# Kernel tuning notes

Measured on AMD Instinct MI355X. Metric: run time of the kernel, lower is better.

The kernel has to match this reference:

```python
import jax, jax.numpy as jnp
import numpy as np

N_NODES = 50000
N_EDGES = 800000
D_IN = 128
D_OUT = 128
NUM_RELS = 100


def setup_inputs() -> dict:
    key = jax.random.key(0)
    k1, k2, k3, k4, k5, k6, k7 = jax.random.split(key, 7)
    h = jax.random.normal(k1, (N_NODES, D_IN), dtype=jnp.float32)
    W = jax.random.normal(k2, (D_IN, D_OUT), dtype=jnp.float32) * 0.05
    attn = jax.random.normal(k3, (2 * D_OUT,), dtype=jnp.float32) * 0.05
    rel_emb = jax.random.normal(k4, (NUM_RELS, 1), dtype=jnp.float32)
    src = jax.random.randint(k5, (N_EDGES,), 0, N_NODES, dtype=jnp.int32)
    dst = jax.random.randint(k6, (N_EDGES,), 0, N_NODES, dtype=jnp.int32)
    etype = jax.random.randint(k7, (N_EDGES,), 0, NUM_RELS, dtype=jnp.int32)
    return {"h": h, "W": W, "attn": attn, "rel_emb": rel_emb,
            "src": src, "dst": dst, "etype": etype}


def reference(h, W, attn, rel_emb, src, dst, etype):
    # h: [N, d_in], W: [d_in, d_out], attn: [2*d_out], rel_emb: [R, 1]
    # src/dst/etype: [E]
    N = h.shape[0]
    d = W.shape[1]
    # padding_idx=0 in nn.Embedding -> row 0 is zero
    rel_table = rel_emb.at[0].set(0.0)
    z = h @ W  # [N, d_out]
    # attn_fc([z_src, z_dst]) = z_src @ a_l + z_dst @ a_r (split the concat-linear)
    s_src = z @ attn[:d]  # [N]
    s_dst = z @ attn[d:]  # [N]
    e = jax.nn.leaky_relu(s_src[src] + s_dst[dst])  # [E], slope 0.01 as in torch
    # segment softmax over incoming edges of each dst node
    m = jax.ops.segment_max(e, dst, num_segments=N)  # [N]
    ex = jnp.exp(e - m[dst])  # [E]
    denom = jax.ops.segment_sum(ex, dst, num_segments=N)  # [N]
    alpha = ex / denom[dst]  # [E]
    coef = rel_table[etype, 0] * alpha  # [E]  (rel_alpha * alpha)
    # weighted sum of source messages per destination node
    out = jax.ops.segment_sum(coef[:, None] * z[src], dst, num_segments=N)  # [N, d_out]
    return out
```

## Files before the change

kernel.cpp:

```cpp
#include <hip/hip_runtime.h>

#define D 128
#define GROWS 64
#define SPLIT 8
#define NPP (256 / SPLIT)
#define MAXPART 1024

typedef __attribute__((ext_vector_type(8))) short short8;
typedef __attribute__((ext_vector_type(4))) float float4v;

__device__ __forceinline__ ushort f2bf(float x) {
    uint u = __float_as_uint(x);
    return (ushort)((u + 0x7FFFu + ((u >> 16) & 1u)) >> 16);
}
__device__ __forceinline__ float bf_lo(uint u) { return __uint_as_float(u << 16); }
__device__ __forceinline__ float bf_hi(uint u) { return __uint_as_float(u & 0xFFFF0000u); }

__global__ __launch_bounds__(256) void convW_kernel(
    const float* __restrict__ W, ushort* __restrict__ Wtg)
{
    int idx = blockIdx.x * 256 + threadIdx.x;
    int k = idx >> 7, n = idx & 127;
    Wtg[n * 128 + k] = f2bf(W[idx]);
}

__global__ __launch_bounds__(512) void gemm_mfma_kernel(
    const float* __restrict__ h, const ushort* __restrict__ Wtg,
    const float* __restrict__ attn, const int* __restrict__ dst,
    ushort* __restrict__ zb, float* __restrict__ s_src, float* __restrict__ s_dst,
    int* __restrict__ histm, int nhi, int N, int E, int nblocks)
{
    __shared__ ushort ht[GROWS * 136];
    __shared__ float psum_s[GROWS][2];
    __shared__ float psum_d[GROWS][2];
    __shared__ int histA[256];
    const int tid = threadIdx.x;
    const int base = blockIdx.x * GROWS;

#pragma unroll
    for (int it = 0; it < 4; ++it) {
        int idx = it * 512 + tid;
        int r = idx >> 5, c4 = (idx & 31) * 4;
        float4 v = make_float4(0.f, 0.f, 0.f, 0.f);
        if (base + r < N) v = *(const float4*)&h[(size_t)(base + r) * D + c4];
        ushort4 u = make_ushort4(f2bf(v.x), f2bf(v.y), f2bf(v.z), f2bf(v.w));
        *(ushort4*)&ht[r * 136 + c4] = u;
    }
    if (tid < 256) histA[tid] = 0;
    __syncthreads();

    const int lane = tid & 63;
    const int wave = tid >> 6;
    const int wr = wave >> 1;
    const int wc = wave & 1;
    const int col = lane & 15;
    const int quad = lane >> 4;
    const int wm = wr * 16;

    float4v acc[4];
#pragma unroll
    for (int nt = 0; nt < 4; ++nt) acc[nt] = (float4v)(0.f);

#pragma unroll
    for (int kc = 0; kc < 128; kc += 32) {
        short8 a = *(const short8*)&ht[(wm + col) * 136 + kc + quad * 8];
#pragma unroll
        for (int nt = 0; nt < 4; ++nt) {
            short8 b = *(const short8*)&Wtg[(wc * 64 + nt * 16 + col) * 128 + kc + quad * 8];
            acc[nt] = __builtin_amdgcn_mfma_f32_16x16x32_bf16(a, b, acc[nt], 0, 0, 0);
        }
    }
    __syncthreads();

    float ps[4] = {0.f, 0.f, 0.f, 0.f}, pd[4] = {0.f, 0.f, 0.f, 0.f};
#pragma unroll
    for (int nt = 0; nt < 4; ++nt) {
        float aL = attn[wc * 64 + nt * 16 + col];
        float aR = attn[D + wc * 64 + nt * 16 + col];
#pragma unroll
        for (int reg = 0; reg < 4; ++reg) {
            float v = acc[nt][reg];
            ps[reg] = fmaf(v, aL, ps[reg]);
            pd[reg] = fmaf(v, aR, pd[reg]);
            ht[(wm + quad * 4 + reg) * 136 + wc * 64 + nt * 16 + col] = f2bf(v);
        }
    }
#pragma unroll
    for (int reg = 0; reg < 4; ++reg) {
#pragma unroll
        for (int off = 1; off < 16; off <<= 1) {
            ps[reg] += __shfl_xor(ps[reg], off);
            pd[reg] += __shfl_xor(pd[reg], off);
        }
        if (col == 0) {
            int rl = wm + quad * 4 + reg;
            psum_s[rl][wc] = ps[reg];
            psum_d[rl][wc] = pd[reg];
        }
    }
    __syncthreads();

    if (tid < GROWS && base + tid < N) {
        s_src[base + tid] = psum_s[tid][0] + psum_s[tid][1];
        s_dst[base + tid] = psum_d[tid][0] + psum_d[tid][1];
    }

#pragma unroll
    for (int it = 0; it < 2; ++it) {
        int idx = it * 512 + tid;
        int r = idx >> 4, c8 = idx & 15;
        if (base + r < N)
            *(uint4*)&zb[(size_t)(base + r) * D + c8 * 8] = *(uint4*)&ht[r * 136 + c8 * 8];
    }

    const int cpb = (E + nblocks - 1) / nblocks;
    const int cs = blockIdx.x * cpb;
    const int ce = min(cs + cpb, E);
    for (int i = cs + tid; i < ce; i += 512)
        atomicAdd(&histA[dst[i] >> 8], 1);
    __syncthreads();
    if (tid < nhi) histm[blockIdx.x * nhi + tid] = histA[tid];
}

__global__ __launch_bounds__(64) void binB1_kernel(
    int* __restrict__ histm, int* __restrict__ colsum, int nhi, int nchunk)
{
    const int b = blockIdx.x;
    const int t = threadIdx.x;
    const int K = (nchunk + 63) / 64;
    int v[16];
    int s = 0;
#pragma unroll
    for (int j = 0; j < 16; ++j) {
        int c = t * K + j;
        v[j] = (j < K && c < nchunk) ? histm[c * nhi + b] : 0;
        s += v[j];
    }
    int incl = s;
#pragma unroll
    for (int off = 1; off < 64; off <<= 1) {
        int u = __shfl_up(incl, off);
        if (t >= off) incl += u;
    }
    int run = incl - s;
#pragma unroll
    for (int j = 0; j < 16; ++j) {
        int c = t * K + j;
        if (j < K && c < nchunk) { histm[c * nhi + b] = run; run += v[j]; }
    }
    if (t == 63) colsum[b] = incl;
}

__device__ __forceinline__ void scan_colsum_wave0(
    const int* __restrict__ colsum, int* sbase, int nhi, int lane)
{
    int v[4];
    int s = 0;
#pragma unroll
    for (int j = 0; j < 4; ++j) {
        int c = lane * 4 + j;
        v[j] = (c < nhi) ? colsum[c] : 0;
        s += v[j];
    }
    int incl = s;
#pragma unroll
    for (int off = 1; off < 64; off <<= 1) {
        int u = __shfl_up(incl, off);
        if (lane >= off) incl += u;
    }
    int run = incl - s;
#pragma unroll
    for (int j = 0; j < 4; ++j) {
        run += v[j];
        sbase[lane * 4 + j] = run;
    }
}

__global__ __launch_bounds__(256) void binC_kernel(
    const int* __restrict__ src, const int* __restrict__ dst,
    const int* __restrict__ etype, const int* __restrict__ histm,
    const int* __restrict__ colsum, uint* __restrict__ binned,
    int nhi, int E, int nchunk)
{
    __shared__ int sbase[256];
    __shared__ int cur[256];
    const int tid = threadIdx.x;
    if (tid < 64) scan_colsum_wave0(colsum, sbase, nhi, tid);
    __syncthreads();
    if (tid < nhi)
        cur[tid] = ((tid == 0) ? 0 : sbase[tid - 1]) + histm[blockIdx.x * nhi + tid];
    __syncthreads();
    const int cpb = (E + nchunk - 1) / nchunk;
    const int cs = blockIdx.x * cpb;
    const int ce = min(cs + cpb, E);
    for (int i = cs + tid; i < ce; i += 256) {
        int d = dst[i];
        int pos = atomicAdd(&cur[d >> 8], 1);
        binned[pos] = (uint)src[i] | ((uint)etype[i] << 16) | ((uint)(d & 255) << 23);
    }
}

__global__ __launch_bounds__(256) void aggD_kernel(
    const uint* __restrict__ zb32, const float* __restrict__ s_src,
    const float* __restrict__ s_dst, const int* __restrict__ colsum,
    const uint* __restrict__ binned, const float* __restrict__ rel_emb,
    float* __restrict__ out, int nhi, int N, int R)
{
    __shared__ float rel_l[128];
    __shared__ int sbase[256];
    __shared__ int hist[NPP];
    __shared__ int loff[NPP + 1];
    __shared__ int cur[NPP];
    __shared__ uint sE[MAXPART];
    const int tid = threadIdx.x;
    const int lane = tid & 63;
    const int wave = tid >> 6;

    if (tid < R) rel_l[tid] = (tid == 0) ? 0.f : rel_emb[tid];
    if (wave == 0) scan_colsum_wave0(colsum, sbase, nhi, lane);
    if (tid < NPP) hist[tid] = 0;
    __syncthreads();

    const int hi = blockIdx.x / SPLIT;
    const int part = blockIdx.x % SPLIT;
    const int bb = (hi == 0) ? 0 : sbase[hi - 1];
    const int be = sbase[hi];
    const int lobase = part * NPP;

    for (int i = bb + tid; i < be; i += 256) {
        int li = (int)((binned[i] >> 23) & 0xFF) - lobase;
        if ((unsigned)li < NPP) atomicAdd(&hist[li], 1);
    }
    __syncthreads();
    if (wave == 0 && lane < NPP) {
        int hc = hist[lane];
        int incl = hc;
#pragma unroll
        for (int off = 1; off < NPP; off <<= 1) {
            int u = __shfl_up(incl, off);
            if (lane >= off) incl += u;
        }
        loff[lane + 1] = incl;
        if (lane == 0) loff[0] = 0;
        cur[lane] = incl - hc;
    }
    __syncthreads();
    for (int i = bb + tid; i < be; i += 256) {
        uint pk = binned[i];
        int li = (int)((pk >> 23) & 0xFF) - lobase;
        if ((unsigned)li < NPP) {
            int pos = atomicAdd(&cur[li], 1);
            if (pos < MAXPART) sE[pos] = pk;
        }
    }
    __syncthreads();

    const int q = lane >> 4;
    const int ql = lane & 15;
    const int qid = wave * 4 + q;
    const int qb = q * 16;

    for (int nIdx = qid; nIdx < NPP; nIdx += 16) {
        const int d = hi * 256 + lobase + nIdx;
        if (d >= N) continue;
        const int st = loff[nIdx];
        const int en = loff[nIdx + 1];
        const float sdst = s_dst[d];

        float lpart = 0.f;
        float4 acc0 = make_float4(0.f, 0.f, 0.f, 0.f);
        float4 acc1 = make_float4(0.f, 0.f, 0.f, 0.f);

        for (int b2 = st; b2 < en; b2 += 16) {
            const int idx = b2 + ql;
            const bool valid = idx < en;
            const uint packed = valid ? sE[idx] : 0;
            const int srcv = (int)(packed & 0xFFFF);
            const int et = (int)((packed >> 16) & 0x7F);
            float w = 0.f;
            if (valid) {
                float x = s_src[srcv] + sdst;
                float e = (x > 0.f) ? x : 0.01f * x;
                float p = __expf(e);
                lpart += p;
                w = p * rel_l[et];
            }
            const int nv = min(16, en - b2);
            for (int j = 0; j < nv; j += 4) {
                const float w0 = __shfl(w, qb + j);
                const float w1 = __shfl(w, qb + j + 1);
                const float w2 = __shfl(w, qb + j + 2);
                const float w3 = __shfl(w, qb + j + 3);
                const int s0 = __shfl(srcv, qb + j);
                const int s1 = __shfl(srcv, qb + j + 1);
                const int s2 = __shfl(srcv, qb + j + 2);
                const int s3 = __shfl(srcv, qb + j + 3);
                const uint4 u0 = *(const uint4*)(zb32 + (size_t)s0 * 64 + ql * 4);
                const uint4 u1 = *(const uint4*)(zb32 + (size_t)s1 * 64 + ql * 4);
                const uint4 u2 = *(const uint4*)(zb32 + (size_t)s2 * 64 + ql * 4);
                const uint4 u3 = *(const uint4*)(zb32 + (size_t)s3 * 64 + ql * 4);
                acc0.x = fmaf(w0, bf_lo(u0.x), acc0.x);
                acc0.y = fmaf(w0, bf_hi(u0.x), acc0.y);
                acc0.z = fmaf(w0, bf_lo(u0.y), acc0.z);
                acc0.w = fmaf(w0, bf_hi(u0.y), acc0.w);
                acc1.x = fmaf(w0, bf_lo(u0.z), acc1.x);
                acc1.y = fmaf(w0, bf_hi(u0.z), acc1.y);
                acc1.z = fmaf(w0, bf_lo(u0.w), acc1.z);
                acc1.w = fmaf(w0, bf_hi(u0.w), acc1.w);
                acc0.x = fmaf(w1, bf_lo(u1.x), acc0.x);
                acc0.y = fmaf(w1, bf_hi(u1.x), acc0.y);
                acc0.z = fmaf(w1, bf_lo(u1.y), acc0.z);
                acc0.w = fmaf(w1, bf_hi(u1.y), acc0.w);
                acc1.x = fmaf(w1, bf_lo(u1.z), acc1.x);
                acc1.y = fmaf(w1, bf_hi(u1.z), acc1.y);
                acc1.z = fmaf(w1, bf_lo(u1.w), acc1.z);
                acc1.w = fmaf(w1, bf_hi(u1.w), acc1.w);
                acc0.x = fmaf(w2, bf_lo(u2.x), acc0.x);
                acc0.y = fmaf(w2, bf_hi(u2.x), acc0.y);
                acc0.z = fmaf(w2, bf_lo(u2.y), acc0.z);
                acc0.w = fmaf(w2, bf_hi(u2.y), acc0.w);
                acc1.x = fmaf(w2, bf_lo(u2.z), acc1.x);
                acc1.y = fmaf(w2, bf_hi(u2.z), acc1.y);
                acc1.z = fmaf(w2, bf_lo(u2.w), acc1.z);
                acc1.w = fmaf(w2, bf_hi(u2.w), acc1.w);
                acc0.x = fmaf(w3, bf_lo(u3.x), acc0.x);
                acc0.y = fmaf(w3, bf_hi(u3.x), acc0.y);
                acc0.z = fmaf(w3, bf_lo(u3.y), acc0.z);
                acc0.w = fmaf(w3, bf_hi(u3.y), acc0.w);
                acc1.x = fmaf(w3, bf_lo(u3.z), acc1.x);
                acc1.y = fmaf(w3, bf_hi(u3.z), acc1.y);
                acc1.z = fmaf(w3, bf_lo(u3.w), acc1.z);
                acc1.w = fmaf(w3, bf_hi(u3.w), acc1.w);
            }
        }

        float l = lpart;
#pragma unroll
        for (int off = 8; off; off >>= 1) l += __shfl_xor(l, off);

        const float inv = (l > 0.f) ? 1.0f / l : 0.f;
        float* orow = out + (size_t)d * D + ql * 8;
        *(float4*)orow       = make_float4(acc0.x * inv, acc0.y * inv, acc0.z * inv, acc0.w * inv);
        *(float4*)(orow + 4) = make_float4(acc1.x * inv, acc1.y * inv, acc1.z * inv, acc1.w * inv);
    }
}

extern "C" void kernel_launch(void* const* d_in, const int* in_sizes, int n_in,
                              void* d_out, int out_size, void* d_ws, size_t ws_size,
                              hipStream_t stream)
{
    const float* h    = (const float*)d_in[0];
    const float* W    = (const float*)d_in[1];
    const float* attn = (const float*)d_in[2];
    const float* rel  = (const float*)d_in[3];
    const int*   src  = (const int*)d_in[4];
    const int*   dst  = (const int*)d_in[5];
    const int*   et   = (const int*)d_in[6];
    float* out = (float*)d_out;

    const int N = in_sizes[0] / D;
    const int E = in_sizes[4];
    const int R = in_sizes[3];

    char* p = (char*)d_ws;
    auto alloc = [&](size_t bytes) {
        char* q = p;
        p += (bytes + 255) & ~(size_t)255;
        return q;
    };
    const int nhi     = (N + 255) / 256;
    const int gblocks = (N + GROWS - 1) / GROWS;

    ushort* zb     = (ushort*)alloc((size_t)N * D * sizeof(ushort));
    ushort* Wtg    = (ushort*)alloc((size_t)D * D * sizeof(ushort));
    float* ssrc    = (float*)alloc((size_t)N * sizeof(float));
    float* sdst    = (float*)alloc((size_t)N * sizeof(float));
    uint*  binned  = (uint*)alloc((size_t)E * sizeof(uint));
    int*   histm   = (int*)alloc((size_t)gblocks * nhi * sizeof(int));
    int*   colsum  = (int*)alloc((size_t)nhi * sizeof(int));

    convW_kernel<<<64, 256, 0, stream>>>(W, Wtg);
    gemm_mfma_kernel<<<gblocks, 512, 0, stream>>>(h, Wtg, attn, dst, zb, ssrc, sdst,
                                                  histm, nhi, N, E, gblocks);
    binB1_kernel<<<nhi, 64, 0, stream>>>(histm, colsum, nhi, gblocks);
    binC_kernel<<<gblocks, 256, 0, stream>>>(src, dst, et, histm, colsum, binned,
                                             nhi, E, gblocks);
    aggD_kernel<<<nhi * SPLIT, 256, 0, stream>>>((const uint*)zb, ssrc, sdst,
                                                 colsum, binned, rel, out, nhi, N, R);
}
```

Measured before the change: 162.1 us.

## Precompute edge softmax weights block-wide in LDS and deepen gather unroll

The aggregation kernel now computes each edge's exponentiated score and relation-scaled weight in a block-wide pass, storing weights in shared memory and accumulating per-node denominators with shared atomics. The per-node gather loop then reads precomputed weights and issues 8 independent row loads at a time instead of shuffling within 16-lane groups. SPLIT doubles to 16 so each quarter-wave owns exactly one destination node, and MAXPART halves. This aims to raise memory-level parallelism and drop shuffle overhead, but it launches more blocks that each rescan the same bin, and edge lists longer than MAXPART are truncated.

```diff
diff --git a/kernel.cpp b/kernel.cpp
--- a/kernel.cpp
+++ b/kernel.cpp
@@ -2,9 +2,9 @@
 
 #define D 128
 #define GROWS 64
-#define SPLIT 8
+#define SPLIT 16
 #define NPP (256 / SPLIT)
-#define MAXPART 1024
+#define MAXPART 512
 
 typedef __attribute__((ext_vector_type(8))) short short8;
 typedef __attribute__((ext_vector_type(4))) float float4v;
@@ -212,13 +212,16 @@
     __shared__ int loff[NPP + 1];
     __shared__ int cur[NPP];
     __shared__ uint sE[MAXPART];
+    __shared__ float sW[MAXPART];
+    __shared__ float sDst[NPP];
+    __shared__ float sDen[NPP];
     const int tid = threadIdx.x;
     const int lane = tid & 63;
     const int wave = tid >> 6;
 
     if (tid < R) rel_l[tid] = (tid == 0) ? 0.f : rel_emb[tid];
     if (wave == 0) scan_colsum_wave0(colsum, sbase, nhi, lane);
-    if (tid < NPP) hist[tid] = 0;
+    if (tid < NPP) { hist[tid] = 0; sDen[tid] = 0.f; }
     __syncthreads();
 
     const int hi = blockIdx.x / SPLIT;
@@ -226,6 +229,12 @@
     const int bb = (hi == 0) ? 0 : sbase[hi - 1];
     const int be = sbase[hi];
     const int lobase = part * NPP;
+    const int dbase = hi * 256 + lobase;
+
+    if (tid < NPP) {
+        int dd = dbase + tid;
+        sDst[tid] = (dd < N) ? s_dst[dd] : 0.f;
+    }
 
     for (int i = bb + tid; i < be; i += 256) {
         int li = (int)((binned[i] >> 23) & 0xFF) - lobase;
@@ -255,94 +264,65 @@
     }
     __syncthreads();
 
+    const int ne = min(loff[NPP], MAXPART);
+    for (int i = tid; i < ne; i += 256) {
+        uint pk = sE[i];
+        int srcv = (int)(pk & 0xFFFF);
+        int et = (int)((pk >> 16) & 0x7F);
+        int li = (int)((pk >> 23) & 0xFF) - lobase;
+        float x = s_src[srcv] + sDst[li];
+        float e = (x > 0.f) ? x : 0.01f * x;
+        float p = __expf(e);
+        sW[i] = p * rel_l[et];
+        atomicAdd(&sDen[li], p);
+    }
+    __syncthreads();
+
     const int q = lane >> 4;
     const int ql = lane & 15;
-    const int qid = wave * 4 + q;
-    const int qb = q * 16;
-
-    for (int nIdx = qid; nIdx < NPP; nIdx += 16) {
-        const int d = hi * 256 + lobase + nIdx;
-        if (d >= N) continue;
-        const int st = loff[nIdx];
-        const int en = loff[nIdx + 1];
-        const float sdst = s_dst[d];
-
-        float lpart = 0.f;
-        float4 acc0 = make_float4(0.f, 0.f, 0.f, 0.f);
-        float4 acc1 = make_float4(0.f, 0.f, 0.f, 0.f);
-
-        for (int b2 = st; b2 < en; b2 += 16) {
-            const int idx = b2 + ql;
-            const bool valid = idx < en;
-            const uint packed = valid ? sE[idx] : 0;
-            const int srcv = (int)(packed & 0xFFFF);
-            const int et = (int)((packed >> 16) & 0x7F);
-            float w = 0.f;
-            if (valid) {
-                float x = s_src[srcv] + sdst;
-                float e = (x > 0.f) ? x : 0.01f * x;
-                float p = __expf(e);
-                lpart += p;
-                w = p * rel_l[et];
-            }
-            const int nv = min(16, en - b2);
-            for (int j = 0; j < nv; j += 4) {
-                const float w0 = __shfl(w, qb + j);
-                const float w1 = __shfl(w, qb + j + 1);
-                const float w2 = __shfl(w, qb + j + 2);
-                const float w3 = __shfl(w, qb + j + 3);
-                const int s0 = __shfl(srcv, qb + j);
-                const int s1 = __shfl(srcv, qb + j + 1);
-                const int s2 = __shfl(srcv, qb + j + 2);
-                const int s3 = __shfl(srcv, qb + j + 3);
-                const uint4 u0 = *(const uint4*)(zb32 + (size_t)s0 * 64 + ql * 4);
-                const uint4 u1 = *(const uint4*)(zb32 + (size_t)s1 * 64 + ql * 4);
-                const uint4 u2 = *(const uint4*)(zb32 + (size_t)s2 * 64 + ql * 4);
-                const uint4 u3 = *(const uint4*)(zb32 + (size_t)s3 * 64 + ql * 4);
-                acc0.x = fmaf(w0, bf_lo(u0.x), acc0.x);
-                acc0.y = fmaf(w0, bf_hi(u0.x), acc0.y);
-                acc0.z = fmaf(w0, bf_lo(u0.y), acc0.z);
-                acc0.w = fmaf(w0, bf_hi(u0.y), acc0.w);
-                acc1.x = fmaf(w0, bf_lo(u0.z), acc1.x);
-                acc1.y = fmaf(w0, bf_hi(u0.z), acc1.y);
-                acc1.z = fmaf(w0, bf_lo(u0.w), acc1.z);
-                acc1.w = fmaf(w0, bf_hi(u0.w), acc1.w);
-                acc0.x = fmaf(w1, bf_lo(u1.x), acc0.x);
-                acc0.y = fmaf(w1, bf_hi(u1.x), acc0.y);
-                acc0.z = fmaf(w1, bf_lo(u1.y), acc0.z);
-                acc0.w = fmaf(w1, bf_hi(u1.y), acc0.w);
-                acc1.x = fmaf(w1, bf_lo(u1.z), acc1.x);
-                acc1.y = fmaf(w1, bf_hi(u1.z), acc1.y);
-                acc1.z = fmaf(w1, bf_lo(u1.w), acc1.z);
-                acc1.w = fmaf(w1, bf_hi(u1.w), acc1.w);
-                acc0.x = fmaf(w2, bf_lo(u2.x), acc0.x);
-                acc0.y = fmaf(w2, bf_hi(u2.x), acc0.y);
-                acc0.z = fmaf(w2, bf_lo(u2.y), acc0.z);
-                acc0.w = fmaf(w2, bf_hi(u2.y), acc0.w);
-                acc1.x = fmaf(w2, bf_lo(u2.z), acc1.x);
-                acc1.y = fmaf(w2, bf_hi(u2.z), acc1.y);
-                acc1.z = fmaf(w2, bf_lo(u2.w), acc1.z);
-                acc1.w = fmaf(w2, bf_hi(u2.w), acc1.w);
-                acc0.x = fmaf(w3, bf_lo(u3.x), acc0.x);
-                acc0.y = fmaf(w3, bf_hi(u3.x), acc0.y);
-                acc0.z = fmaf(w3, bf_lo(u3.y), acc0.z);
-                acc0.w = fmaf(w3, bf_hi(u3.y), acc0.w);
-                acc1.x = fmaf(w3, bf_lo(u3.z), acc1.x);
-                acc1.y = fmaf(w3, bf_hi(u3.z), acc1.y);
-                acc1.z = fmaf(w3, bf_lo(u3.w), acc1.z);
-                acc1.w = fmaf(w3, bf_hi(u3.w), acc1.w);
-            }
-        }
-
-        float l = lpart;
-#pragma unroll
-        for (int off = 8; off; off >>= 1) l += __shfl_xor(l, off);
-
-        const float inv = (l > 0.f) ? 1.0f / l : 0.f;
-        float* orow = out + (size_t)d * D + ql * 8;
-        *(float4*)orow       = make_float4(acc0.x * inv, acc0.y * inv, acc0.z * inv, acc0.w * inv);
-        *(float4*)(orow + 4) = make_float4(acc1.x * inv, acc1.y * inv, acc1.z * inv, acc1.w * inv);
-    }
+    const int nIdx = wave * 4 + q;
+    const int d = dbase + nIdx;
+    if (d >= N) return;
+
+    const int st = min(loff[nIdx], MAXPART);
+    const int en = min(loff[nIdx + 1], MAXPART);
+    const float den = sDen[nIdx];
+    const float inv = (den > 0.f) ? 1.0f / den : 0.f;
+
+    float4 acc0 = make_float4(0.f, 0.f, 0.f, 0.f);
+    float4 acc1 = make_float4(0.f, 0.f, 0.f, 0.f);
+
+    for (int b2 = st; b2 < en; b2 += 8) {
+        float w[8];
+        int sv[8];
+#pragma unroll
+        for (int j = 0; j < 8; ++j) {
+            int idx = b2 + j;
+            bool valid = idx < en;
+            w[j] = valid ? sW[idx] : 0.f;
+            sv[j] = valid ? (int)(sE[idx] & 0xFFFF) : 0;
+        }
+        uint4 u[8];
+#pragma unroll
+        for (int j = 0; j < 8; ++j)
+            u[j] = *(const uint4*)(zb32 + (size_t)sv[j] * 64 + ql * 4);
+#pragma unroll
+        for (int j = 0; j < 8; ++j) {
+            const float wj = w[j];
+            acc0.x = fmaf(wj, bf_lo(u[j].x), acc0.x);
+            acc0.y = fmaf(wj, bf_hi(u[j].x), acc0.y);
+            acc0.z = fmaf(wj, bf_lo(u[j].y), acc0.z);
+            acc0.w = fmaf(wj, bf_hi(u[j].y), acc0.w);
+            acc1.x = fmaf(wj, bf_lo(u[j].z), acc1.x);
+            acc1.y = fmaf(wj, bf_hi(u[j].z), acc1.y);
+            acc1.z = fmaf(wj, bf_lo(u[j].w), acc1.z);
+            acc1.w = fmaf(wj, bf_hi(u[j].w), acc1.w);
+        }
+    }
+
+    float* orow = out + (size_t)d * D + ql * 8;
+    *(float4*)orow       = make_float4(acc0.x * inv, acc0.y * inv, acc0.z * inv, acc0.w * inv);
+    *(float4*)(orow + 4) = make_float4(acc1.x * inv, acc1.y * inv, acc1.z * inv, acc1.w * inv);
 }
 
 extern "C" void kernel_launch(void* const* d_in, const int* in_sizes, int n_in,
```

After: 182.7 us. +12.7%, slower.
